# Kernel tuning notes

Hardware: AMD Instinct MI355X
Metric: run time of the kernel (lower is better)

Reference implementation:

```python
import jax, jax.numpy as jnp
import numpy as np

EMBED_DIM = 1024
NUM_HEADS = 16
HEAD_DIM = EMBED_DIM // NUM_HEADS
BATCH = 2
SEQ = 2048


def setup_inputs() -> dict:
    key = jax.random.key(0)
    ks = jax.random.split(key, 9)
    s = EMBED_DIM ** -0.5
    inp = {"x": jax.random.normal(ks[0], (BATCH, SEQ, EMBED_DIM), dtype=jnp.float32)}
    names = ["Wq", "Wk", "Wv", "Wo"]
    for i, n in enumerate(names):
        inp[n] = jax.random.normal(ks[1 + i], (EMBED_DIM, EMBED_DIM), dtype=jnp.float32) * s
        inp["b" + n[1]] = jax.random.normal(ks[5 + i], (EMBED_DIM,), dtype=jnp.float32) * 0.02
    return inp


def reference(x, Wq, bq, Wk, bk, Wv, bv, Wo, bo):
    B, S, E = x.shape
    H, D = NUM_HEADS, HEAD_DIM
    scaling = D ** -0.5
    # projections (torch Linear: x @ W.T + b), reshape to (B, H, S, D)
    q = (x @ Wq.T + bq).reshape(B, S, H, D).transpose(0, 2, 1, 3)
    k = (x @ Wk.T + bk).reshape(B, S, H, D).transpose(0, 2, 1, 3)
    v = (x @ Wv.T + bv).reshape(B, S, H, D).transpose(0, 2, 1, 3)
    # full materialized score matrix, matching the original module
    scores = jnp.einsum("bhqd,bhkd->bhqk", q, k) * scaling
    causal = jnp.triu(jnp.ones((S, S), dtype=bool), k=1)  # True above diagonal
    scores = jnp.where(causal[None, None], -jnp.inf, scores)
    attn = jax.nn.softmax(scores, axis=-1)
    out = jnp.einsum("bhqk,bhkd->bhqd", attn, v)  # (B, H, S, D)
    out = out.transpose(0, 2, 1, 3).reshape(B, S, E)
    return out @ Wo.T + bo
```

## Files before the change

### kernel.cpp

```cpp
#include <hip/hip_runtime.h>
#include <stdint.h>

typedef __bf16 bf16;
typedef __bf16 bf16x8 __attribute__((ext_vector_type(8)));
typedef __bf16 bf16x4 __attribute__((ext_vector_type(4)));
typedef float  f32x4  __attribute__((ext_vector_type(4)));
typedef unsigned int u32;

#define E_DIM 1024
#define S_LEN 2048
#define BATCH 2
#define NH 16
#define DH 64

#define NEG_INF (-__builtin_inff())

union BU { u32 u[4]; bf16x8 h; };

__device__ __forceinline__ u32 cvtpk_bf16(float lo, float hi) {
    u32 r;
    asm("v_cvt_pk_bf16_f32 %0, %1, %2" : "=v"(r) : "v"(lo), "v"(hi));
    return r;
}
__device__ __forceinline__ void pswap32(u32 &a, u32 &b) {
    asm("v_permlane32_swap_b32 %0, %1" : "+v"(a), "+v"(b));
}
__device__ __forceinline__ void pswap16(u32 &a, u32 &b) {
    asm("v_permlane16_swap_b32 %0, %1" : "+v"(a), "+v"(b));
}
__device__ __forceinline__ float fast_exp2(float x) {
    float r;
    asm("v_exp_f32 %0, %1" : "=v"(r) : "v"(x));
    return r;
}

__device__ __forceinline__ void load_lds16(const bf16* g, bf16* l) {
    __builtin_amdgcn_global_load_lds(
        (const __attribute__((address_space(1))) void*)g,
        (__attribute__((address_space(3))) void*)l, 16, 0, 0);
}

__global__ __launch_bounds__(256) void convert_kernel(
    const float* __restrict__ s0, const float* __restrict__ s1,
    const float* __restrict__ s2, const float* __restrict__ s3,
    const float* __restrict__ s4,
    bf16* __restrict__ d0, bf16* __restrict__ d1, bf16* __restrict__ d2,
    bf16* __restrict__ d3, bf16* __restrict__ d4,
    int n0, int n1)
{
    const float* src; bf16* dst; int n;
    switch (blockIdx.y) {
        case 0:  src = s0; dst = d0; n = n0; break;
        case 1:  src = s1; dst = d1; n = n1; break;
        case 2:  src = s2; dst = d2; n = n1; break;
        case 3:  src = s3; dst = d3; n = n1; break;
        default: src = s4; dst = d4; n = n1; break;
    }
    int i = (blockIdx.x * 256 + threadIdx.x) * 4;
    if (i >= n) return;
    float4 v = *(const float4*)(src + i);
    bf16x4 o;
    o[0] = (bf16)v.x; o[1] = (bf16)v.y; o[2] = (bf16)v.z; o[3] = (bf16)v.w;
    *(bf16x4*)(dst + i) = o;
}

__global__ __launch_bounds__(256) void gemm_kernel(
    const bf16* __restrict__ A,
    const bf16* __restrict__ W,
    const float* __restrict__ bias0, const float* __restrict__ bias1,
    const float* __restrict__ bias2,
    bf16* __restrict__ outQ, bf16* __restrict__ outK, bf16* __restrict__ outVt,
    float* __restrict__ outF, int final_mode)
{
    __shared__ bf16 As[2][128 * 32];
    __shared__ bf16 Bs[2][128 * 32];

    const int bid = blockIdx.x;
    const int xcd = bid & 7, idx = bid >> 3;
    int mtile, ntile;
    if (final_mode) {
        mtile = (xcd >> 1) * 8 + (idx >> 2);
        ntile = (xcd & 1) * 4 + (idx & 3);
    } else {
        mtile = (xcd >> 1) * 8 + idx / 12;
        ntile = (xcd & 1) * 12 + idx % 12;
    }
    const int bm = mtile * 128, bn = ntile * 128;
    const int mode = final_mode ? 3 : (bn >> 10);
    const float* bias = (mode == 1) ? bias1 : (mode == 2 ? bias2 : bias0);

    const int t = threadIdx.x;
    const int lane = t & 63, w = t >> 6;
    const int quad = lane >> 4, l16 = lane & 15;
    const int wm = (w & 1) * 64, wn = (w >> 1) * 64;

    const int r0 = w * 16;
    const int srow = r0 + (lane >> 2), scol = (lane & 3) * 8;
    const bf16* Ag0 = A + (size_t)(bm + srow) * E_DIM + scol;
    const bf16* Ag1 = Ag0 + (size_t)64 * E_DIM;
    const bf16* Wg0 = W + (size_t)(bn + srow) * E_DIM + scol;
    const bf16* Wg1 = Wg0 + (size_t)64 * E_DIM;

    f32x4 acc[4][4];
#pragma unroll
    for (int i = 0; i < 4; i++)
#pragma unroll
        for (int j = 0; j < 4; j++) acc[i][j] = f32x4{0.f, 0.f, 0.f, 0.f};

    load_lds16(Ag0, As[0] + r0 * 32);
    load_lds16(Ag1, As[0] + (64 + r0) * 32);
    load_lds16(Wg0, Bs[0] + r0 * 32);
    load_lds16(Wg1, Bs[0] + (64 + r0) * 32);

    int cur = 0;
    for (int kt = 0; kt < E_DIM; kt += 32) {
        __syncthreads();

        if (kt + 32 < E_DIM) {
            const int nxt = cur ^ 1;
            load_lds16(Ag0 + kt + 32, As[nxt] + r0 * 32);
            load_lds16(Ag1 + kt + 32, As[nxt] + (64 + r0) * 32);
            load_lds16(Wg0 + kt + 32, Bs[nxt] + r0 * 32);
            load_lds16(Wg1 + kt + 32, Bs[nxt] + (64 + r0) * 32);
        }

        bf16x8 af[4], bfr[4];
#pragma unroll
        for (int i = 0; i < 4; i++)
            af[i] = *(const bf16x8*)(As[cur] + (wm + i * 16 + l16) * 32 + quad * 8);
#pragma unroll
        for (int j = 0; j < 4; j++)
            bfr[j] = *(const bf16x8*)(Bs[cur] + (wn + j * 16 + l16) * 32 + quad * 8);
#pragma unroll
        for (int i = 0; i < 4; i++)
#pragma unroll
            for (int j = 0; j < 4; j++)
                acc[i][j] = __builtin_amdgcn_mfma_f32_16x16x32_bf16(af[i], bfr[j], acc[i][j], 0, 0, 0);

        cur ^= 1;
    }

#pragma unroll
    for (int j = 0; j < 4; j++) {
        const int n = bn + wn + j * 16 + l16;
        const int nl = n & 1023;
        const float bv = bias[nl];
#pragma unroll
        for (int i = 0; i < 4; i++) {
            const int m0 = bm + wm + i * 16 + quad * 4;
            if (mode == 3) {
#pragma unroll
                for (int r = 0; r < 4; r++)
                    outF[(size_t)(m0 + r) * E_DIM + nl] = acc[i][j][r] + bv;
            } else if (mode == 2) {
                const int b_ = m0 >> 11, s0 = m0 & (S_LEN - 1);
                const int h = nl >> 6, d = nl & 63;
                bf16x4 pv;
#pragma unroll
                for (int r = 0; r < 4; r++) pv[r] = (bf16)(acc[i][j][r] + bv);
                *(bf16x4*)(outVt + ((size_t)((b_ * NH + h) * DH + d)) * S_LEN + s0) = pv;
            } else {
                bf16* o = (mode == 0) ? outQ : outK;
                const float sc = (mode == 0) ? 0.18033688f : 1.0f;
                const int h = nl >> 6, d = nl & 63;
#pragma unroll
                for (int r = 0; r < 4; r++) {
                    const int m = m0 + r;
                    const int b_ = m >> 11, s = m & (S_LEN - 1);
                    o[((size_t)(b_ * NH + h) * S_LEN + s) * DH + d] = (bf16)((acc[i][j][r] + bv) * sc);
                }
            }
        }
    }
}

__global__ __launch_bounds__(512, 4) void attn_kernel(
    const bf16* __restrict__ Qb, const bf16* __restrict__ Kb,
    const bf16* __restrict__ Vtb,
    float* __restrict__ Opart, float* __restrict__ Lpart)
{
    __shared__ __align__(16) char smem[35840];
    bf16* Ks = (bf16*)smem;
    bf16* Vs = (bf16*)(smem + 18432);

    const int t = threadIdx.x, lane = t & 63, w = t >> 6;
    const int quad = lane >> 4, l16 = lane & 15;
    const int qs = w & 3, kh = w >> 2;

    const int i = blockIdx.x;
    const int xcd = i & 7, idx = i >> 3;
    const int bh  = (xcd << 2) | (idx & 3);
    const int g   = idx >> 2;
    int qt, c0;
    if (g < 4)       { qt = g;                            c0 = 0; }
    else if (g < 12) { int u = g - 4;  qt = 4 + (u >> 1); c0 = u & 1; }
    else if (g < 24) { int u = g - 12; qt = 8 + u / 3;    c0 = u % 3; }
    else             { int u = g - 24; qt = 12 + (u >> 2); c0 = u & 3; }
    const int k0 = c0 * 4;
    const int k1 = (k0 + 3 < qt) ? k0 + 3 : qt;

    const bf16* Qg = Qb + (size_t)bh * S_LEN * DH;
    const bf16* Kg = Kb + (size_t)bh * S_LEN * DH;
    const bf16* Vg = Vtb + (size_t)bh * DH * S_LEN;
    float* Op = Opart + ((size_t)(bh * 16 + qt) * 4 + c0) * (128 * 64);
    float* Lp = Lpart + ((size_t)(bh * 16 + qt) * 4 + c0) * 128;

    const int qrow0 = qt * 128 + qs * 32;

    bf16x8 qf[2][2];
#pragma unroll
    for (int qh = 0; qh < 2; qh++) {
        const bf16* qp = Qg + (size_t)(qrow0 + qh * 16 + l16) * DH + quad * 8;
        qf[qh][0] = *(const bf16x8*)(qp);
        qf[qh][1] = *(const bf16x8*)(qp + 32);
    }

    f32x4 o[2][4];
    f32x4 lacc[2];
#pragma unroll
    for (int qh = 0; qh < 2; qh++) {
        lacc[qh] = f32x4{0.f, 0.f, 0.f, 0.f};
#pragma unroll
        for (int dt = 0; dt < 4; dt++) o[qh][dt] = f32x4{0.f, 0.f, 0.f, 0.f};
    }

    const int kr0 = t >> 3, kce = (t & 7) * 8;
    const int vr0 = t >> 4, vce = (t & 15) * 8;

    const int kb0 = k0 * 128;
    uint4 kA = *(const uint4*)(Kg + (size_t)(kb0 + kr0) * DH + kce);
    uint4 kB = *(const uint4*)(Kg + (size_t)(kb0 + kr0 + 64) * DH + kce);
    uint4 vA = *(const uint4*)(Vg + (size_t)vr0 * S_LEN + kb0 + vce);
    uint4 vB = *(const uint4*)(Vg + (size_t)(vr0 + 32) * S_LEN + kb0 + vce);

    for (int kt = k0; kt <= k1; kt++) {
        __syncthreads();
        *(uint4*)(Ks + kr0 * 72 + kce) = kA;
        *(uint4*)(Ks + (kr0 + 64) * 72 + kce) = kB;
        *(uint4*)(Vs + vr0 * 136 + vce) = vA;
        *(uint4*)(Vs + (vr0 + 32) * 136 + vce) = vB;
        __syncthreads();

        if (kt < k1) {
            const int kb = (kt + 1) * 128;
            kA = *(const uint4*)(Kg + (size_t)(kb + kr0) * DH + kce);
            kB = *(const uint4*)(Kg + (size_t)(kb + kr0 + 64) * DH + kce);
            vA = *(const uint4*)(Vg + (size_t)vr0 * S_LEN + kb + vce);
            vB = *(const uint4*)(Vg + (size_t)(vr0 + 32) * S_LEN + kb + vce);
        }

        const bool diag = (kt == qt);

#pragma unroll
        for (int itp = 0; itp < 2; itp++) {
            f32x4 p[2][2];
#pragma unroll
            for (int e = 0; e < 2; e++) {
                const int itg = kh * 4 + itp * 2 + e;
                const bf16* kp = Ks + (itg * 16 + l16) * 72 + quad * 8;
                bf16x8 kf0 = *(const bf16x8*)(kp);
                bf16x8 kf1 = *(const bf16x8*)(kp + 32);
#pragma unroll
                for (int qh = 0; qh < 2; qh++) {
                    f32x4 s = __builtin_amdgcn_mfma_f32_16x16x32_bf16(
                        kf0, qf[qh][0], f32x4{0.f, 0.f, 0.f, 0.f}, 0, 0, 0);
                    s = __builtin_amdgcn_mfma_f32_16x16x32_bf16(
                        kf1, qf[qh][1], s, 0, 0, 0);
                    if (diag) {
                        const int kloc = kh * 64 + (itp * 2 + e) * 16 + quad * 4;
                        const int qloc = qs * 32 + qh * 16 + l16;
#pragma unroll
                        for (int r = 0; r < 4; r++)
                            if (kloc + r > qloc) s[r] = NEG_INF;
                    }
                    f32x4 pe;
#pragma unroll
                    for (int r = 0; r < 4; r++) pe[r] = fast_exp2(s[r]);
                    lacc[qh] += pe;
                    p[qh][e] = pe;
                }
            }

            BU bu0, bu1;
            {
                u32 a0 = cvtpk_bf16(p[0][0][0], p[0][0][1]);
                u32 a1 = cvtpk_bf16(p[0][0][2], p[0][0][3]);
                u32 b0 = cvtpk_bf16(p[0][1][0], p[0][1][1]);
                u32 b1 = cvtpk_bf16(p[0][1][2], p[0][1][3]);
                pswap32(a0, b0); pswap16(a0, b0);
                pswap32(a1, b1); pswap16(a1, b1);
                bu0.u[0] = a0; bu0.u[1] = a1; bu0.u[2] = b0; bu0.u[3] = b1;
            }
            {
                u32 a0 = cvtpk_bf16(p[1][0][0], p[1][0][1]);
                u32 a1 = cvtpk_bf16(p[1][0][2], p[1][0][3]);
                u32 b0 = cvtpk_bf16(p[1][1][0], p[1][1][1]);
                u32 b1 = cvtpk_bf16(p[1][1][2], p[1][1][3]);
                pswap32(a0, b0); pswap16(a0, b0);
                pswap32(a1, b1); pswap16(a1, b1);
                bu1.u[0] = a0; bu1.u[1] = a1; bu1.u[2] = b0; bu1.u[3] = b1;
            }

            const int ksg = kh * 2 + itp;
#pragma unroll
            for (int dt = 0; dt < 4; dt++) {
                bf16x8 vf = *(const bf16x8*)(Vs + (dt * 16 + l16) * 136 + ksg * 32 + quad * 8);
                o[0][dt] = __builtin_amdgcn_mfma_f32_16x16x32_bf16(vf, bu0.h, o[0][dt], 0, 0, 0);
                o[1][dt] = __builtin_amdgcn_mfma_f32_16x16x32_bf16(vf, bu1.h, o[1][dt], 0, 0, 0);
            }
        }
    }

    float lsum[2];
#pragma unroll
    for (int qh = 0; qh < 2; qh++) {
        float l = lacc[qh][0] + lacc[qh][1] + lacc[qh][2] + lacc[qh][3];
        l += __shfl_xor(l, 16);
        l += __shfl_xor(l, 32);
        lsum[qh] = l;
    }

    __syncthreads();
    f32x4* Or = (f32x4*)smem;
    float*  Lr = (float*)(smem + 32768);

    if (kh == 1) {
#pragma unroll
        for (int qh = 0; qh < 2; qh++) {
#pragma unroll
            for (int dt = 0; dt < 4; dt++)
                Or[(((qs * 2 + qh) * 4 + dt) * 4 + quad) * 16 + l16] = o[qh][dt];
            if (quad == 0) Lr[(qs * 2 + qh) * 16 + l16] = lsum[qh];
        }
    }
    __syncthreads();
    if (kh == 0) {
#pragma unroll
        for (int qh = 0; qh < 2; qh++) {
            const float lc = lsum[qh] + Lr[(qs * 2 + qh) * 16 + l16];
            const int row = qs * 32 + qh * 16 + l16;
            if (quad == 0) Lp[row] = lc;
#pragma unroll
            for (int dt = 0; dt < 4; dt++) {
                f32x4 ov = o[qh][dt] + Or[(((qs * 2 + qh) * 4 + dt) * 4 + quad) * 16 + l16];
                *(f32x4*)(Op + (size_t)row * 64 + dt * 16 + quad * 4) = ov;
            }
        }
    }
}

__global__ __launch_bounds__(256) void norm_kernel(
    const float* __restrict__ Opart, const float* __restrict__ Lpart,
    bf16* __restrict__ Ab)
{
    const int j = (blockIdx.x * 256 + threadIdx.x) * 4;
    const int b = j >> 21, s = (j >> 10) & (S_LEN - 1), e = j & 1023;
    const int h = e >> 6, d = e & 63;
    const int bh = b * NH + h;
    const int qt = s >> 7, row = s & 127;
    const int nc = (qt >> 2) + 1;
    const float* Op = Opart + ((size_t)(bh * 16 + qt) * 4) * (128 * 64)
                    + (size_t)row * 64 + d;
    const float* Lp = Lpart + ((size_t)(bh * 16 + qt) * 4) * 128 + row;
    f32x4 ov = *(const f32x4*)Op;
    float l = Lp[0];
    for (int c = 1; c < nc; c++) {
        ov += *(const f32x4*)(Op + c * (128 * 64));
        l += Lp[c * 128];
    }
    const float inv = 1.0f / l;
    bf16x4 w4;
#pragma unroll
    for (int r = 0; r < 4; r++) w4[r] = (bf16)(ov[r] * inv);
    *(bf16x4*)(Ab + j) = w4;
}

extern "C" void kernel_launch(void* const* d_in, const int* in_sizes, int n_in,
                              void* d_out, int out_size, void* d_ws, size_t ws_size,
                              hipStream_t stream)
{
    const float* x  = (const float*)d_in[0];
    const float* Wq = (const float*)d_in[1];
    const float* bq = (const float*)d_in[2];
    const float* Wk = (const float*)d_in[3];
    const float* bk = (const float*)d_in[4];
    const float* Wv = (const float*)d_in[5];
    const float* bv = (const float*)d_in[6];
    const float* Wo = (const float*)d_in[7];
    const float* bo = (const float*)d_in[8];
    float* out = (float*)d_out;

    char* ws = (char*)d_ws;
    const size_t MB = 1ull << 20;
    bf16*  xb    = (bf16*)(ws + 0);
    bf16*  wqb   = (bf16*)(ws + 8 * MB);
    bf16*  wkb   = (bf16*)(ws + 10 * MB);
    bf16*  wvb   = (bf16*)(ws + 12 * MB);
    bf16*  wob   = (bf16*)(ws + 14 * MB);
    bf16*  Qb    = (bf16*)(ws + 16 * MB);
    bf16*  Kb    = (bf16*)(ws + 24 * MB);
    bf16*  Vtb   = (bf16*)(ws + 32 * MB);
    bf16*  Ab    = (bf16*)(ws + 40 * MB);
    float* Opart = (float*)(ws + 48 * MB);
    float* Lpart = (float*)(ws + 112 * MB);

    convert_kernel<<<dim3(4096, 5), 256, 0, stream>>>(
        x, Wq, Wk, Wv, Wo, xb, wqb, wkb, wvb, wob, 4194304, 1048576);

    gemm_kernel<<<dim3(768), 256, 0, stream>>>(
        xb, wqb, bq, bk, bv, Qb, Kb, Vtb, nullptr, 0);

    attn_kernel<<<dim3(1280), 512, 0, stream>>>(Qb, Kb, Vtb, Opart, Lpart);

    norm_kernel<<<dim3(4096), 256, 0, stream>>>(Opart, Lpart, Ab);

    gemm_kernel<<<dim3(256), 256, 0, stream>>>(
        Ab, wob, bo, bo, bo, nullptr, nullptr, nullptr, out, 1);
}
```

Baseline: 202.5 us.

## Fuse split-K attention combine into attn kernel via atomic counters; swizzle GEMM LDS

Removes the separate norm kernel. Each attention block now bumps a per-(head, query-tile) atomic counter, and the last chunk to finish sums the partial O and L values, normalizes them and writes bf16 output directly. The counters are zeroed by an extra grid row in the convert kernel. Separately, the GEMM's LDS layout is XOR-swizzled on both the async store and the fragment reads to reduce bank conflicts. This trades one kernel launch and a full pass over the partials for thread fences, an atomic and a serialized tail on the last-finishing blocks.

```diff
diff --git a/kernel.cpp b/kernel.cpp
--- a/kernel.cpp
+++ b/kernel.cpp
@@ -46,8 +46,16 @@
     const float* __restrict__ s4,
     bf16* __restrict__ d0, bf16* __restrict__ d1, bf16* __restrict__ d2,
     bf16* __restrict__ d3, bf16* __restrict__ d4,
+    int* __restrict__ Cnt,
     int n0, int n1)
 {
+    if (blockIdx.y == 5) {
+        if (blockIdx.x == 0) {
+            Cnt[threadIdx.x] = 0;
+            Cnt[threadIdx.x + 256] = 0;
+        }
+        return;
+    }
     const float* src; bf16* dst; int n;
     switch (blockIdx.y) {
         case 0:  src = s0; dst = d0; n = n0; break;
@@ -95,7 +103,8 @@
     const int wm = (w & 1) * 64, wn = (w >> 1) * 64;
 
     const int r0 = w * 16;
-    const int srow = r0 + (lane >> 2), scol = (lane & 3) * 8;
+    const int srow = r0 + (lane >> 2);
+    const int scol = ((lane & 3) ^ ((lane >> 3) & 3)) * 8;
     const bf16* Ag0 = A + (size_t)(bm + srow) * E_DIM + scol;
     const bf16* Ag1 = Ag0 + (size_t)64 * E_DIM;
     const bf16* Wg0 = W + (size_t)(bn + srow) * E_DIM + scol;
@@ -111,6 +120,8 @@
     load_lds16(Ag1, As[0] + (64 + r0) * 32);
     load_lds16(Wg0, Bs[0] + r0 * 32);
     load_lds16(Wg1, Bs[0] + (64 + r0) * 32);
+
+    const int rchunk = (quad ^ ((l16 >> 1) & 3)) * 8;
 
     int cur = 0;
     for (int kt = 0; kt < E_DIM; kt += 32) {
@@ -127,10 +138,10 @@
         bf16x8 af[4], bfr[4];
 #pragma unroll
         for (int i = 0; i < 4; i++)
-            af[i] = *(const bf16x8*)(As[cur] + (wm + i * 16 + l16) * 32 + quad * 8);
+            af[i] = *(const bf16x8*)(As[cur] + (wm + i * 16 + l16) * 32 + rchunk);
 #pragma unroll
         for (int j = 0; j < 4; j++)
-            bfr[j] = *(const bf16x8*)(Bs[cur] + (wn + j * 16 + l16) * 32 + quad * 8);
+            bfr[j] = *(const bf16x8*)(Bs[cur] + (wn + j * 16 + l16) * 32 + rchunk);
 #pragma unroll
         for (int i = 0; i < 4; i++)
 #pragma unroll
@@ -177,9 +188,11 @@
 __global__ __launch_bounds__(512, 4) void attn_kernel(
     const bf16* __restrict__ Qb, const bf16* __restrict__ Kb,
     const bf16* __restrict__ Vtb,
-    float* __restrict__ Opart, float* __restrict__ Lpart)
+    float* __restrict__ Opart, float* __restrict__ Lpart,
+    bf16* __restrict__ Ab, int* __restrict__ Cnt)
 {
     __shared__ __align__(16) char smem[35840];
+    __shared__ int sFlag;
     bf16* Ks = (bf16*)smem;
     bf16* Vs = (bf16*)(smem + 18432);
 
@@ -347,32 +360,33 @@
             }
         }
     }
-}
-
-__global__ __launch_bounds__(256) void norm_kernel(
-    const float* __restrict__ Opart, const float* __restrict__ Lpart,
-    bf16* __restrict__ Ab)
-{
-    const int j = (blockIdx.x * 256 + threadIdx.x) * 4;
-    const int b = j >> 21, s = (j >> 10) & (S_LEN - 1), e = j & 1023;
-    const int h = e >> 6, d = e & 63;
-    const int bh = b * NH + h;
-    const int qt = s >> 7, row = s & 127;
+
+    __threadfence();
+    __syncthreads();
+    if (t == 0) sFlag = atomicAdd(&Cnt[bh * 16 + qt], 1);
+    __syncthreads();
     const int nc = (qt >> 2) + 1;
-    const float* Op = Opart + ((size_t)(bh * 16 + qt) * 4) * (128 * 64)
-                    + (size_t)row * 64 + d;
-    const float* Lp = Lpart + ((size_t)(bh * 16 + qt) * 4) * 128 + row;
-    f32x4 ov = *(const f32x4*)Op;
-    float l = Lp[0];
-    for (int c = 1; c < nc; c++) {
-        ov += *(const f32x4*)(Op + c * (128 * 64));
-        l += Lp[c * 128];
-    }
-    const float inv = 1.0f / l;
-    bf16x4 w4;
-#pragma unroll
-    for (int r = 0; r < 4; r++) w4[r] = (bf16)(ov[r] * inv);
-    *(bf16x4*)(Ab + j) = w4;
+    if (sFlag == nc - 1) {
+        __threadfence();
+        const float* Ob = Opart + ((size_t)(bh * 16 + qt) * 4) * (128 * 64);
+        const float* Lb = Lpart + ((size_t)(bh * 16 + qt) * 4) * 128;
+        bf16* Aq = Ab + ((size_t)(bh >> 4) * S_LEN + (size_t)qt * 128) * E_DIM
+                      + (bh & 15) * DH;
+        for (int task = t; task < 2048; task += 512) {
+            const int row = task >> 4, dc = (task & 15) * 4;
+            float l = Lb[row];
+            f32x4 ov = *(const f32x4*)(Ob + (size_t)row * 64 + dc);
+            for (int c = 1; c < nc; c++) {
+                l += Lb[c * 128 + row];
+                ov += *(const f32x4*)(Ob + (size_t)c * (128 * 64) + (size_t)row * 64 + dc);
+            }
+            const float inv = 1.0f / l;
+            bf16x4 w4;
+#pragma unroll
+            for (int r = 0; r < 4; r++) w4[r] = (bf16)(ov[r] * inv);
+            *(bf16x4*)(Aq + (size_t)row * E_DIM + dc) = w4;
+        }
+    }
 }
 
 extern "C" void kernel_launch(void* const* d_in, const int* in_sizes, int n_in,
@@ -403,16 +417,16 @@
     bf16*  Ab    = (bf16*)(ws + 40 * MB);
     float* Opart = (float*)(ws + 48 * MB);
     float* Lpart = (float*)(ws + 112 * MB);
-
-    convert_kernel<<<dim3(4096, 5), 256, 0, stream>>>(
-        x, Wq, Wk, Wv, Wo, xb, wqb, wkb, wvb, wob, 4194304, 1048576);
+    int*   Cnt   = (int*)(ws + 113 * MB);
+
+    convert_kernel<<<dim3(4096, 6), 256, 0, stream>>>(
+        x, Wq, Wk, Wv, Wo, xb, wqb, wkb, wvb, wob, Cnt, 4194304, 1048576);
 
     gemm_kernel<<<dim3(768), 256, 0, stream>>>(
         xb, wqb, bq, bk, bv, Qb, Kb, Vtb, nullptr, 0);
 
-    attn_kernel<<<dim3(1280), 512, 0, stream>>>(Qb, Kb, Vtb, Opart, Lpart);
-
-    norm_kernel<<<dim3(4096), 256, 0, stream>>>(Opart, Lpart, Ab);
+    attn_kernel<<<dim3(1280), 512, 0, stream>>>(
+        Qb, Kb, Vtb, Opart, Lpart, Ab, Cnt);
 
     gemm_kernel<<<dim3(256), 256, 0, stream>>>(
         Ab, wob, bo, bo, bo, nullptr, nullptr, nullptr, out, 1);
```

Measured after the change: 614.8 us. 3.04x slower.
